# Kernel tuning notes

Hardware: AMD Instinct MI355X
Metric: run time of the kernel (lower is better)

## Reference

```python
import jax, jax.numpy as jnp
import numpy as np
from jax import lax

K_FILTERS = 4
TEMPERATURE = 30.0


def setup_inputs() -> dict:
    key = jax.random.key(0)
    k1, k2, k3, k4 = jax.random.split(key, 4)
    B, C, H, W = 16, 256, 64, 64
    O, Cin, kk = 256, 256, 3
    hidden = int(C * 0.25) + 1  # 65
    x = jax.random.normal(k1, (B, C, H, W), dtype=jnp.float32)
    # kaiming-normal-ish scales for SE 1x1 convs (fan_out, relu)
    fc1_w = jax.random.normal(k2, (hidden, C), dtype=jnp.float32) * np.float32(np.sqrt(2.0 / hidden))
    fc2_w = jax.random.normal(k3, (O * K_FILTERS, hidden), dtype=jnp.float32) * np.float32(np.sqrt(2.0 / (O * K_FILTERS)))
    fc2_b = jnp.zeros((O * K_FILTERS,), dtype=jnp.float32)
    he_std = np.float32(np.sqrt(2.0) * (C * kk * kk) ** (-0.5))
    weight = jax.random.normal(k4, (K_FILTERS, O, Cin, kk, kk), dtype=jnp.float32) * he_std
    return {"x": x, "fc1_w": fc1_w, "fc2_w": fc2_w, "fc2_b": fc2_b, "weight": weight}


def reference(x, fc1_w, fc2_w, fc2_b, weight):
    B, C, H, W = x.shape
    K, O, Cin, kh, kw = weight.shape
    # SE module: global avg pool -> 1x1 conv (fc) -> relu -> 1x1 conv (fc)
    pooled = x.mean(axis=(2, 3))                      # [B, C]
    h = jax.nn.relu(pooled @ fc1_w.T)                 # [B, hidden]
    y = h @ fc2_w.T + fc2_b                           # [B, K*O]
    # softmax over K filters per output channel
    prob = jax.nn.softmax(y.reshape(B, K, O) / TEMPERATURE, axis=1)  # [B, K, O]
    # per-sample aggregated conv weights
    agg = jnp.einsum('bko,kof->bof', prob, weight.reshape(K, O, Cin * kh * kw))
    agg = agg.reshape(B, O, Cin, kh, kw)              # [B, O, Cin, kh, kw]
    # batched conv with per-sample filters (stride=1, padding=1, dilation=1, groups=1)
    def conv_one(xi, wi):
        return lax.conv_general_dilated(
            xi[None], wi, window_strides=(1, 1), padding=[(1, 1), (1, 1)],
            dimension_numbers=('NCHW', 'OIHW', 'NCHW'))[0]
    out = jax.vmap(conv_one)(x, agg)                  # [B, O, H, W]
    return out
```

## Files before the change

### kernel.cpp

```cpp
#include <hip/hip_runtime.h>
#include <hip/hip_bf16.h>
#include <stdint.h>


typedef __bf16 bf16x8 __attribute__((ext_vector_type(8)));
typedef float  f32x4  __attribute__((ext_vector_type(4)));

__device__ __forceinline__ unsigned short f2bf(float f) {
  union { float f; unsigned u; } v; v.f = f;
  return (unsigned short)((v.u + 0x7FFFu + ((v.u >> 16) & 1u)) >> 16);
}

__device__ __forceinline__ void gload16(const void* g, void* l) {
  __builtin_amdgcn_global_load_lds(
      (const __attribute__((address_space(1))) void*)g,
      (__attribute__((address_space(3))) void*)l, 16, 0, 0);
}

#define WAIT_VM(N) do { __builtin_amdgcn_sched_barrier(0); \
  asm volatile("s_waitcnt vmcnt(" #N ")" ::: "memory"); \
  __builtin_amdgcn_sched_barrier(0); } while (0)
#define BARRIER_PIN() do { __builtin_amdgcn_s_barrier(); \
  __builtin_amdgcn_sched_barrier(0); } while (0)

__global__ __launch_bounds__(256) void k_prep(
    const float* __restrict__ x, unsigned short* __restrict__ xn,
    float* __restrict__ pooled_sum) {
  const int bx = blockIdx.x;
  const int y  = bx & 63;
  const int cc = (bx >> 6) & 3;
  const int b  = bx >> 8;
  const int t  = threadIdx.x;
  const int cl = t >> 2;
  const int q  = t & 3;
  const int xs = q * 16;

  const float4* s4 = (const float4*)(x + (((size_t)(b * 256 + cc * 64 + cl) * 64 + y) * 64 + xs));
  float v[16];
#pragma unroll
  for (int i = 0; i < 4; ++i) {
    float4 f = s4[i];
    v[i * 4 + 0] = f.x; v[i * 4 + 1] = f.y; v[i * 4 + 2] = f.z; v[i * 4 + 3] = f.w;
  }
  float s = 0.f;
#pragma unroll
  for (int i = 0; i < 16; ++i) s += v[i];
  s += __shfl_xor(s, 1);
  s += __shfl_xor(s, 2);
  if (q == 0) atomicAdd(&pooled_sum[b * 256 + cc * 64 + cl], s);

  __shared__ unsigned short tile[64][72];
#pragma unroll
  for (int j = 0; j < 16; ++j) tile[xs + j][cl] = f2bf(v[j]);
  __syncthreads();
  const int xp = t >> 2;
  const uint4* ls = (const uint4*)&tile[xp][q * 16];
  uint4 a0 = ls[0], a1 = ls[1];
  uint4* gd = (uint4*)(xn + ((size_t)((b * 64 + y) * 64 + xp) * 256 + cc * 64 + q * 16));
  gd[0] = a0; gd[1] = a1;
}

__global__ __launch_bounds__(256) void k_fc(
    const float* __restrict__ pooled_sum,
    const float* __restrict__ fc1, const float* __restrict__ fc2,
    const float* __restrict__ fc2b, float* __restrict__ prob) {
  const int b = blockIdx.x, t = threadIdx.x;
  __shared__ float p[256];
  __shared__ float h[72];
  __shared__ float yv[1024];
  p[t] = pooled_sum[b * 256 + t] * (1.0f / 4096.0f);
  __syncthreads();
  if (t < 65) {
    float s = 0.f;
    for (int c = 0; c < 256; ++c) s += p[c] * fc1[t * 256 + c];
    h[t] = fmaxf(s, 0.f);
  }
  __syncthreads();
  for (int m = t; m < 1024; m += 256) {
    float s = fc2b[m];
    for (int j = 0; j < 65; ++j) s += h[j] * fc2[m * 65 + j];
    yv[m] = s;
  }
  __syncthreads();
  const float invT = 1.0f / 30.0f;
  float e0 = yv[t] * invT, e1 = yv[256 + t] * invT, e2 = yv[512 + t] * invT, e3 = yv[768 + t] * invT;
  float mx = fmaxf(fmaxf(e0, e1), fmaxf(e2, e3));
  float x0 = expf(e0 - mx), x1 = expf(e1 - mx), x2 = expf(e2 - mx), x3 = expf(e3 - mx);
  float r = 1.0f / (x0 + x1 + x2 + x3);
  prob[(b * 4 + 0) * 256 + t] = x0 * r;
  prob[(b * 4 + 1) * 256 + t] = x1 * r;
  prob[(b * 4 + 2) * 256 + t] = x2 * r;
  prob[(b * 4 + 3) * 256 + t] = x3 * r;
}

__global__ __launch_bounds__(256) void k_agg(
    const float* __restrict__ weight, const float* __restrict__ prob,
    unsigned short* __restrict__ aggT) {
  const int o = blockIdx.x, t = threadIdx.x;
  __shared__ float w[4][2304];
#pragma unroll
  for (int k = 0; k < 4; ++k) {
    const float4* src = (const float4*)(weight + (size_t)(k * 256 + o) * 2304);
    float4* dst = (float4*)w[k];
    for (int j = t; j < 576; j += 256) dst[j] = src[j];
  }
  __syncthreads();
  const int c = t;
  float wv[4][9];
#pragma unroll
  for (int k = 0; k < 4; ++k)
#pragma unroll
    for (int tap = 0; tap < 9; ++tap) wv[k][tap] = w[k][c * 9 + tap];
  for (int b = 0; b < 16; ++b) {
    float p0 = prob[(b * 4 + 0) * 256 + o];
    float p1 = prob[(b * 4 + 1) * 256 + o];
    float p2 = prob[(b * 4 + 2) * 256 + o];
    float p3 = prob[(b * 4 + 3) * 256 + o];
#pragma unroll
    for (int tap = 0; tap < 9; ++tap) {
      float vv = p0 * wv[0][tap] + p1 * wv[1][tap] + p2 * wv[2][tap] + p3 * wv[3][tap];
      aggT[((size_t)(b * 9 + tap) * 256 + o) * 256 + c] = f2bf(vv);
    }
  }
}

__global__ __launch_bounds__(256, 2) void k_conv(
    const unsigned short* __restrict__ xn,
    const unsigned short* __restrict__ aggT,
    const unsigned short* __restrict__ zpage,
    float* __restrict__ out) {
  const int bx0 = blockIdx.x;
  const int bx  = (bx0 & 7) * 128 + (bx0 >> 3);
  const int ot = bx & 1;
  const int yt = (bx >> 1) & 31;
  const int b  = bx >> 6;
  const int y0 = yt * 2;
  const int o0 = ot * 128;
  const int t    = threadIdx.x;
  const int lane = t & 63;
  const int l15  = lane & 15;
  const int lg   = lane >> 4;
  const int wid  = t >> 6;
  const int wm   = wid >> 1;
  const int wn   = wid & 1;

  __shared__ unsigned short xbuf[256 * 64];
  __shared__ unsigned short wbuf[3][128 * 64];

  const f32x4 vzero = {0.f, 0.f, 0.f, 0.f};
  const bf16x8 bzero = {};
  f32x4 acc[4][4];
#pragma unroll
  for (int i = 0; i < 4; ++i)
#pragma unroll
    for (int j = 0; j < 4; ++j) acc[i][j] = vzero;

  const unsigned short* xb = xn + (size_t)b * (64 * 64 * 256);
  const unsigned short* ab = aggT + (size_t)b * (9 * 256 * 256) + (size_t)o0 * 256;

  for (int cc = 0; cc < 4; ++cc) {
    const int c0 = cc * 64;
#pragma unroll
    for (int i = 0; i < 8; ++i) {
      int u = t + i * 256;
      int pos = u >> 3, s = u & 7;
      int rr = pos >> 6, xc = pos & 63;
      int yy = y0 - 1 + rr;
      int sp = (s ^ (pos & 7)) * 8;
      const unsigned short* src = (yy >= 0 && yy < 64)
          ? xb + ((size_t)yy * 64 + xc) * 256 + (c0 + sp)
          : zpage + ((u & 127) * 8);
      gload16(src, &xbuf[u * 8]);
    }
#pragma unroll
    for (int tp = 0; tp < 2; ++tp) {
      unsigned short* dst = wbuf[tp];
      const unsigned short* wsrc = ab + (size_t)tp * (256 * 256) + c0;
#pragma unroll
      for (int i = 0; i < 4; ++i) {
        int u = t + i * 256;
        int o = u >> 3, s = u & 7;
        gload16(wsrc + (size_t)o * 256 + ((s ^ (o & 7)) * 8), &dst[u * 8]);
      }
    }
    WAIT_VM(4);
    BARRIER_PIN();

#pragma unroll
    for (int tap = 0; tap < 9; ++tap) {
      if (tap < 7) {
        unsigned short* dst = wbuf[(tap + 2) % 3];
        const unsigned short* wsrc = ab + (size_t)(tap + 2) * (256 * 256) + c0;
#pragma unroll
        for (int i = 0; i < 4; ++i) {
          int u = t + i * 256;
          int o = u >> 3, s = u & 7;
          gload16(wsrc + (size_t)o * 256 + ((s ^ (o & 7)) * 8), &dst[u * 8]);
        }
      }
      const int kh = tap / 3;
      const int d  = tap % 3 - 1;
      const int prow = (wm + kh) * 64;
      const unsigned short* wb = wbuf[tap % 3];
#pragma unroll
      for (int ku = 0; ku < 2; ++ku) {
        bf16x8 av[4], bv[4];
#pragma unroll
        for (int mf = 0; mf < 4; ++mf) {
          int xsrc = mf * 16 + l15 + d;
          bool valid = (xsrc >= 0) && (xsrc < 64);
          int xcl = min(max(xsrc, 0), 63);
          int pos = prow + xcl;
          int su = (ku * 4 + lg) ^ (pos & 7);
          av[mf] = *(const bf16x8*)&xbuf[pos * 64 + su * 8];
          if (!valid) av[mf] = bzero;
        }
#pragma unroll
        for (int nf = 0; nf < 4; ++nf) {
          int oo = wn * 64 + nf * 16 + l15;
          int su = (ku * 4 + lg) ^ (oo & 7);
          bv[nf] = *(const bf16x8*)&wb[oo * 64 + su * 8];
        }
        __builtin_amdgcn_s_setprio(1);
#pragma unroll
        for (int mf = 0; mf < 4; ++mf)
#pragma unroll
          for (int nf = 0; nf < 4; ++nf)
            acc[mf][nf] = __builtin_amdgcn_mfma_f32_16x16x32_bf16(av[mf], bv[nf], acc[mf][nf], 0, 0, 0);
        __builtin_amdgcn_s_setprio(0);
      }
      if (tap < 7) { WAIT_VM(4); } else { WAIT_VM(0); }
      BARRIER_PIN();
    }
  }

  const int yrow = y0 + wm;
#pragma unroll
  for (int nf = 0; nf < 4; ++nf) {
    int och = o0 + wn * 64 + nf * 16 + l15;
    float* op = out + ((size_t)(b * 256 + och) * 4096) + yrow * 64;
#pragma unroll
    for (int mf = 0; mf < 4; ++mf) {
      int xcb = mf * 16 + lg * 4;
      *(float4*)(op + xcb) = *(float4*)&acc[mf][nf];
    }
  }
}

extern "C" void kernel_launch(void* const* d_in, const int* in_sizes, int n_in,
                              void* d_out, int out_size, void* d_ws, size_t ws_size,
                              hipStream_t stream) {
  (void)in_sizes; (void)n_in; (void)out_size; (void)ws_size;
  const float* x      = (const float*)d_in[0];
  const float* fc1    = (const float*)d_in[1];
  const float* fc2    = (const float*)d_in[2];
  const float* fc2b   = (const float*)d_in[3];
  const float* weight = (const float*)d_in[4];
  float* out = (float*)d_out;

  char* ws = (char*)d_ws;
  unsigned short* zpage  = (unsigned short*)ws;
  float*          pooled = (float*)(ws + 4096);
  float*          prob   = (float*)(ws + 20480);
  unsigned short* aggT   = (unsigned short*)(ws + 131072);
  unsigned short* xnhwc  = (unsigned short*)(ws + 131072 + 18874368);

  hipMemsetAsync(d_ws, 0, 20480, stream);
  k_prep<<<dim3(16 * 4 * 64), dim3(256), 0, stream>>>(x, xnhwc, pooled);
  k_fc  <<<dim3(16),          dim3(256), 0, stream>>>(pooled, fc1, fc2, fc2b, prob);
  k_agg <<<dim3(256),         dim3(256), 0, stream>>>(weight, prob, aggT);
  k_conv<<<dim3(1024),        dim3(256), 0, stream>>>(xnhwc, aggT, zpage, out);
}
```

Measured before the change: 133.0 us.

## Load conv weights directly to registers and double-buffer x tiles; widen prep blocks

The conv kernel no longer stages per-tap weight tiles through LDS. Each wave reads its B fragments straight from global memory into registers, double-buffered across taps, and the x tile is double-buffered in LDS across channel chunks so one barrier per chunk replaces one per tap. The prep kernel now handles all 256 channels per block, packing bf16 pairs into a wider LDS tile and cutting the block count and atomics per block. This trades LDS traffic and barriers for more register pressure and for uncoalesced direct global loads of weights that may not be hidden behind the MFMAs.

```diff
diff --git a/kernel.cpp b/kernel.cpp
--- a/kernel.cpp
+++ b/kernel.cpp
@@ -17,8 +17,8 @@
       (__attribute__((address_space(3))) void*)l, 16, 0, 0);
 }
 
-#define WAIT_VM(N) do { __builtin_amdgcn_sched_barrier(0); \
-  asm volatile("s_waitcnt vmcnt(" #N ")" ::: "memory"); \
+#define WAIT_VM0() do { __builtin_amdgcn_sched_barrier(0); \
+  asm volatile("s_waitcnt vmcnt(0)" ::: "memory"); \
   __builtin_amdgcn_sched_barrier(0); } while (0)
 #define BARRIER_PIN() do { __builtin_amdgcn_s_barrier(); \
   __builtin_amdgcn_sched_barrier(0); } while (0)
@@ -28,36 +28,37 @@
     float* __restrict__ pooled_sum) {
   const int bx = blockIdx.x;
   const int y  = bx & 63;
-  const int cc = (bx >> 6) & 3;
-  const int b  = bx >> 8;
+  const int b  = bx >> 6;
   const int t  = threadIdx.x;
-  const int cl = t >> 2;
-  const int q  = t & 3;
-  const int xs = q * 16;
-
-  const float4* s4 = (const float4*)(x + (((size_t)(b * 256 + cc * 64 + cl) * 64 + y) * 64 + xs));
-  float v[16];
-#pragma unroll
-  for (int i = 0; i < 4; ++i) {
-    float4 f = s4[i];
-    v[i * 4 + 0] = f.x; v[i * 4 + 1] = f.y; v[i * 4 + 2] = f.z; v[i * 4 + 3] = f.w;
-  }
-  float s = 0.f;
-#pragma unroll
-  for (int i = 0; i < 16; ++i) s += v[i];
-  s += __shfl_xor(s, 1);
-  s += __shfl_xor(s, 2);
-  if (q == 0) atomicAdd(&pooled_sum[b * 256 + cc * 64 + cl], s);
-
-  __shared__ unsigned short tile[64][72];
-#pragma unroll
-  for (int j = 0; j < 16; ++j) tile[xs + j][cl] = f2bf(v[j]);
-  __syncthreads();
-  const int xp = t >> 2;
-  const uint4* ls = (const uint4*)&tile[xp][q * 16];
-  uint4 a0 = ls[0], a1 = ls[1];
-  uint4* gd = (uint4*)(xn + ((size_t)((b * 64 + y) * 64 + xp) * 256 + cc * 64 + q * 16));
-  gd[0] = a0; gd[1] = a1;
+  const int c2 = t & 127;
+  const int xh = t >> 7;
+
+  const float4* r0 = (const float4*)(x + (((size_t)(b * 256 + 2 * c2    ) * 64 + y) * 64 + xh * 32));
+  const float4* r1 = (const float4*)(x + (((size_t)(b * 256 + 2 * c2 + 1) * 64 + y) * 64 + xh * 32));
+
+  __shared__ unsigned int tile[64][132];
+
+  float s0 = 0.f, s1 = 0.f;
+#pragma unroll
+  for (int i = 0; i < 8; ++i) {
+    float4 a0 = r0[i], a1 = r1[i];
+    s0 += a0.x + a0.y + a0.z + a0.w;
+    s1 += a1.x + a1.y + a1.z + a1.w;
+    const int xb = xh * 32 + i * 4;
+    tile[xb + 0][c2] = (unsigned)f2bf(a0.x) | ((unsigned)f2bf(a1.x) << 16);
+    tile[xb + 1][c2] = (unsigned)f2bf(a0.y) | ((unsigned)f2bf(a1.y) << 16);
+    tile[xb + 2][c2] = (unsigned)f2bf(a0.z) | ((unsigned)f2bf(a1.z) << 16);
+    tile[xb + 3][c2] = (unsigned)f2bf(a0.w) | ((unsigned)f2bf(a1.w) << 16);
+  }
+  atomicAdd(&pooled_sum[b * 256 + 2 * c2    ], s0);
+  atomicAdd(&pooled_sum[b * 256 + 2 * c2 + 1], s1);
+  __syncthreads();
+
+  const int p = t >> 2, q = t & 3;
+  const uint4* ls = (const uint4*)&tile[p][q * 32];
+  uint4* gd = (uint4*)(xn + ((size_t)((b * 64 + y) * 64 + p) * 256 + q * 64));
+#pragma unroll
+  for (int i = 0; i < 8; ++i) gd[i] = ls[i];
 }
 
 __global__ __launch_bounds__(256) void k_fc(
@@ -144,8 +145,7 @@
   const int wm   = wid >> 1;
   const int wn   = wid & 1;
 
-  __shared__ unsigned short xbuf[256 * 64];
-  __shared__ unsigned short wbuf[3][128 * 64];
+  __shared__ unsigned short xbuf[2][256 * 64];
 
   const f32x4 vzero = {0.f, 0.f, 0.f, 0.f};
   const bf16x8 bzero = {};
@@ -157,9 +157,10 @@
 
   const unsigned short* xb = xn + (size_t)b * (64 * 64 * 256);
   const unsigned short* ab = aggT + (size_t)b * (9 * 256 * 256) + (size_t)o0 * 256;
-
-  for (int cc = 0; cc < 4; ++cc) {
-    const int c0 = cc * 64;
+  const unsigned short* wbase = ab + (size_t)(wn * 64 + l15) * 256 + lg * 8;
+
+  auto stageX = [&](int buf, int cc) {
+    const int c0s = cc * 64;
 #pragma unroll
     for (int i = 0; i < 8; ++i) {
       int u = t + i * 256;
@@ -168,43 +169,47 @@
       int yy = y0 - 1 + rr;
       int sp = (s ^ (pos & 7)) * 8;
       const unsigned short* src = (yy >= 0 && yy < 64)
-          ? xb + ((size_t)yy * 64 + xc) * 256 + (c0 + sp)
+          ? xb + ((size_t)yy * 64 + xc) * 256 + (c0s + sp)
           : zpage + ((u & 127) * 8);
-      gload16(src, &xbuf[u * 8]);
-    }
-#pragma unroll
-    for (int tp = 0; tp < 2; ++tp) {
-      unsigned short* dst = wbuf[tp];
-      const unsigned short* wsrc = ab + (size_t)tp * (256 * 256) + c0;
-#pragma unroll
-      for (int i = 0; i < 4; ++i) {
-        int u = t + i * 256;
-        int o = u >> 3, s = u & 7;
-        gload16(wsrc + (size_t)o * 256 + ((s ^ (o & 7)) * 8), &dst[u * 8]);
-      }
-    }
-    WAIT_VM(4);
-    BARRIER_PIN();
+      gload16(src, &xbuf[buf][u * 8]);
+    }
+  };
+
+  stageX(0, 0);
+  WAIT_VM0();
+  BARRIER_PIN();
+
+  for (int cc = 0; cc < 4; ++cc) {
+    const int c0 = cc * 64;
+    const unsigned short* xcur = xbuf[cc & 1];
+    if (cc < 3) {
+      stageX((cc + 1) & 1, cc + 1);
+      __builtin_amdgcn_sched_barrier(0);
+    }
+
+    bf16x8 bfrag[2][8];
+#pragma unroll
+    for (int nf = 0; nf < 4; ++nf)
+#pragma unroll
+      for (int ku = 0; ku < 2; ++ku)
+        bfrag[0][nf * 2 + ku] = *(const bf16x8*)(wbase + nf * 4096 + c0 + ku * 32);
 
 #pragma unroll
     for (int tap = 0; tap < 9; ++tap) {
-      if (tap < 7) {
-        unsigned short* dst = wbuf[(tap + 2) % 3];
-        const unsigned short* wsrc = ab + (size_t)(tap + 2) * (256 * 256) + c0;
-#pragma unroll
-        for (int i = 0; i < 4; ++i) {
-          int u = t + i * 256;
-          int o = u >> 3, s = u & 7;
-          gload16(wsrc + (size_t)o * 256 + ((s ^ (o & 7)) * 8), &dst[u * 8]);
-        }
+      if (tap < 8) {
+        const unsigned short* wt = wbase + (size_t)(tap + 1) * 65536 + c0;
+#pragma unroll
+        for (int nf = 0; nf < 4; ++nf)
+#pragma unroll
+          for (int ku = 0; ku < 2; ++ku)
+            bfrag[(tap + 1) & 1][nf * 2 + ku] = *(const bf16x8*)(wt + nf * 4096 + ku * 32);
       }
       const int kh = tap / 3;
       const int d  = tap % 3 - 1;
       const int prow = (wm + kh) * 64;
-      const unsigned short* wb = wbuf[tap % 3];
 #pragma unroll
       for (int ku = 0; ku < 2; ++ku) {
-        bf16x8 av[4], bv[4];
+        bf16x8 av[4];
 #pragma unroll
         for (int mf = 0; mf < 4; ++mf) {
           int xsrc = mf * 16 + l15 + d;
@@ -212,26 +217,21 @@
           int xcl = min(max(xsrc, 0), 63);
           int pos = prow + xcl;
           int su = (ku * 4 + lg) ^ (pos & 7);
-          av[mf] = *(const bf16x8*)&xbuf[pos * 64 + su * 8];
+          av[mf] = *(const bf16x8*)&xcur[pos * 64 + su * 8];
           if (!valid) av[mf] = bzero;
         }
-#pragma unroll
-        for (int nf = 0; nf < 4; ++nf) {
-          int oo = wn * 64 + nf * 16 + l15;
-          int su = (ku * 4 + lg) ^ (oo & 7);
-          bv[nf] = *(const bf16x8*)&wb[oo * 64 + su * 8];
-        }
         __builtin_amdgcn_s_setprio(1);
 #pragma unroll
         for (int mf = 0; mf < 4; ++mf)
 #pragma unroll
           for (int nf = 0; nf < 4; ++nf)
-            acc[mf][nf] = __builtin_amdgcn_mfma_f32_16x16x32_bf16(av[mf], bv[nf], acc[mf][nf], 0, 0, 0);
+            acc[mf][nf] = __builtin_amdgcn_mfma_f32_16x16x32_bf16(
+                av[mf], bfrag[tap & 1][nf * 2 + ku], acc[mf][nf], 0, 0, 0);
         __builtin_amdgcn_s_setprio(0);
       }
-      if (tap < 7) { WAIT_VM(4); } else { WAIT_VM(0); }
-      BARRIER_PIN();
-    }
+    }
+    WAIT_VM0();
+    BARRIER_PIN();
   }
 
   const int yrow = y0 + wm;
@@ -266,8 +266,8 @@
   unsigned short* xnhwc  = (unsigned short*)(ws + 131072 + 18874368);
 
   hipMemsetAsync(d_ws, 0, 20480, stream);
-  k_prep<<<dim3(16 * 4 * 64), dim3(256), 0, stream>>>(x, xnhwc, pooled);
-  k_fc  <<<dim3(16),          dim3(256), 0, stream>>>(pooled, fc1, fc2, fc2b, prob);
-  k_agg <<<dim3(256),         dim3(256), 0, stream>>>(weight, prob, aggT);
-  k_conv<<<dim3(1024),        dim3(256), 0, stream>>>(xnhwc, aggT, zpage, out);
-}
+  k_prep<<<dim3(16 * 64),  dim3(256), 0, stream>>>(x, xnhwc, pooled);
+  k_fc  <<<dim3(16),       dim3(256), 0, stream>>>(pooled, fc1, fc2, fc2b, prob);
+  k_agg <<<dim3(256),      dim3(256), 0, stream>>>(weight, prob, aggT);
+  k_conv<<<dim3(1024),     dim3(256), 0, stream>>>(xnhwc, aggT, zpage, out);
+}
```

New measurement: 220.2 us. 65.6% more time.

## Software-pipeline LDS fragment reads ahead of MFMAs across taps and channel chunks

Applied to the files above, without the earlier changes.

Restructures the conv main loop so that the A and B fragments for the next tap are read from LDS while the current tap's MFMAs run, holding all 8 fragments per operand in registers. It also prefetches the next channel chunk's x tile and the first weight taps across the chunk boundary, so the pipeline does not drain and refill at the start of each chunk. The aim is to hide LDS read latency and the per-chunk prologue stalls. In exchange it uses more registers and relies on delicate waitcnt and barrier ordering: the x buffer is overwritten while tap-8 reads are still pending, guarded by an extra lgkmcnt wait and barrier.

```diff
diff --git a/kernel.cpp b/kernel.cpp
--- a/kernel.cpp
+++ b/kernel.cpp
@@ -21,6 +21,8 @@
   asm volatile("s_waitcnt vmcnt(" #N ")" ::: "memory"); \
   __builtin_amdgcn_sched_barrier(0); } while (0)
 #define BARRIER_PIN() do { __builtin_amdgcn_s_barrier(); \
+  __builtin_amdgcn_sched_barrier(0); } while (0)
+#define LGKM0_PIN() do { asm volatile("s_waitcnt lgkmcnt(0)" ::: "memory"); \
   __builtin_amdgcn_sched_barrier(0); } while (0)
 
 __global__ __launch_bounds__(256) void k_prep(
@@ -158,8 +160,18 @@
   const unsigned short* xb = xn + (size_t)b * (64 * 64 * 256);
   const unsigned short* ab = aggT + (size_t)b * (9 * 256 * 256) + (size_t)o0 * 256;
 
-  for (int cc = 0; cc < 4; ++cc) {
-    const int c0 = cc * 64;
+  auto stage_w = [&](int tap, int ccs) {
+    unsigned short* dst = wbuf[tap % 3];
+    const unsigned short* wsrc = ab + (size_t)tap * (256 * 256) + ccs * 64;
+#pragma unroll
+    for (int i = 0; i < 4; ++i) {
+      int u = t + i * 256;
+      int o = u >> 3, s = u & 7;
+      gload16(wsrc + (size_t)o * 256 + ((s ^ (o & 7)) * 8), &dst[u * 8]);
+    }
+  };
+  auto stage_x = [&](int ccs) {
+    const int c0s = ccs * 64;
 #pragma unroll
     for (int i = 0; i < 8; ++i) {
       int u = t + i * 256;
@@ -168,71 +180,99 @@
       int yy = y0 - 1 + rr;
       int sp = (s ^ (pos & 7)) * 8;
       const unsigned short* src = (yy >= 0 && yy < 64)
-          ? xb + ((size_t)yy * 64 + xc) * 256 + (c0 + sp)
+          ? xb + ((size_t)yy * 64 + xc) * 256 + (c0s + sp)
           : zpage + ((u & 127) * 8);
       gload16(src, &xbuf[u * 8]);
     }
-#pragma unroll
-    for (int tp = 0; tp < 2; ++tp) {
-      unsigned short* dst = wbuf[tp];
-      const unsigned short* wsrc = ab + (size_t)tp * (256 * 256) + c0;
-#pragma unroll
-      for (int i = 0; i < 4; ++i) {
-        int u = t + i * 256;
-        int o = u >> 3, s = u & 7;
-        gload16(wsrc + (size_t)o * 256 + ((s ^ (o & 7)) * 8), &dst[u * 8]);
-      }
-    }
-    WAIT_VM(4);
-    BARRIER_PIN();
-
+  };
+
+#define READ_A1(I, KU, MF, TAP) do {                                    \
+    const int kh_ = (TAP) / 3, d_ = (TAP) % 3 - 1;                      \
+    int xsrc_ = (MF) * 16 + l15 + d_;                                   \
+    bool valid_ = (xsrc_ >= 0) && (xsrc_ < 64);                         \
+    int pos_ = (wm + kh_) * 64 + min(max(xsrc_, 0), 63);                \
+    int su_ = ((KU) * 4 + lg) ^ (pos_ & 7);                             \
+    bf16x8 v_ = *(const bf16x8*)&xbuf[pos_ * 64 + su_ * 8];             \
+    av[I] = valid_ ? v_ : bzero;                                        \
+  } while (0)
+#define READ_A_ALL(TAP) do {                                            \
+    READ_A1(0, 0, 0, TAP); READ_A1(1, 0, 1, TAP);                       \
+    READ_A1(2, 0, 2, TAP); READ_A1(3, 0, 3, TAP);                       \
+    READ_A1(4, 1, 0, TAP); READ_A1(5, 1, 1, TAP);                       \
+    READ_A1(6, 1, 2, TAP); READ_A1(7, 1, 3, TAP);                       \
+  } while (0)
+#define READ_B1(I, KU, NF, SLOT) do {                                   \
+    int oo_ = wn * 64 + (NF) * 16 + l15;                                \
+    int su_ = ((KU) * 4 + lg) ^ (oo_ & 7);                              \
+    bv[I] = *(const bf16x8*)&wbuf[SLOT][oo_ * 64 + su_ * 8];            \
+  } while (0)
+#define READ_B_ALL(SLOT) do {                                           \
+    READ_B1(0, 0, 0, SLOT); READ_B1(1, 0, 1, SLOT);                     \
+    READ_B1(2, 0, 2, SLOT); READ_B1(3, 0, 3, SLOT);                     \
+    READ_B1(4, 1, 0, SLOT); READ_B1(5, 1, 1, SLOT);                     \
+    READ_B1(6, 1, 2, SLOT); READ_B1(7, 1, 3, SLOT);                     \
+  } while (0)
+#define MFMA4(AI, KU, MF) do {                                          \
+    acc[MF][0] = __builtin_amdgcn_mfma_f32_16x16x32_bf16(av[AI], bv[(KU)*4+0], acc[MF][0], 0, 0, 0); \
+    acc[MF][1] = __builtin_amdgcn_mfma_f32_16x16x32_bf16(av[AI], bv[(KU)*4+1], acc[MF][1], 0, 0, 0); \
+    acc[MF][2] = __builtin_amdgcn_mfma_f32_16x16x32_bf16(av[AI], bv[(KU)*4+2], acc[MF][2], 0, 0, 0); \
+    acc[MF][3] = __builtin_amdgcn_mfma_f32_16x16x32_bf16(av[AI], bv[(KU)*4+3], acc[MF][3], 0, 0, 0); \
+  } while (0)
+#define MFMA_ALL() do {                                                 \
+    __builtin_amdgcn_s_setprio(1);                                      \
+    MFMA4(0, 0, 0); MFMA4(1, 0, 1); MFMA4(2, 0, 2); MFMA4(3, 0, 3);     \
+    MFMA4(4, 1, 0); MFMA4(5, 1, 1); MFMA4(6, 1, 2); MFMA4(7, 1, 3);     \
+    __builtin_amdgcn_s_setprio(0);                                      \
+  } while (0)
+
+  bf16x8 av[8], bv[8];
+
+  stage_x(0);
+  stage_w(0, 0);
+  stage_w(1, 0);
+  WAIT_VM(4);
+  BARRIER_PIN();
+  READ_B_ALL(0);
+  READ_A_ALL(0);
+
+  for (int cc = 0; cc < 4; ++cc) {
 #pragma unroll
     for (int tap = 0; tap < 9; ++tap) {
+      if (tap == 8 && cc < 3) stage_x(cc + 1);
+      if (cc < 3 || tap <= 6) stage_w((tap + 2) % 9, cc + (tap + 2) / 9);
+
+      MFMA_ALL();
+
       if (tap < 7) {
-        unsigned short* dst = wbuf[(tap + 2) % 3];
-        const unsigned short* wsrc = ab + (size_t)(tap + 2) * (256 * 256) + c0;
-#pragma unroll
-        for (int i = 0; i < 4; ++i) {
-          int u = t + i * 256;
-          int o = u >> 3, s = u & 7;
-          gload16(wsrc + (size_t)o * 256 + ((s ^ (o & 7)) * 8), &dst[u * 8]);
+        READ_A_ALL(tap + 1);
+        WAIT_VM(4);
+        BARRIER_PIN();
+        READ_B_ALL((tap + 1) % 3);
+      } else if (tap == 7) {
+        READ_A_ALL(8);
+        if (cc < 3) { WAIT_VM(4); } else { WAIT_VM(0); }
+        BARRIER_PIN();
+        READ_B_ALL(2);
+        if (cc < 3) {
+          LGKM0_PIN();
+          BARRIER_PIN();
+        }
+      } else {
+        if (cc < 3) {
+          WAIT_VM(4);
+          BARRIER_PIN();
+          READ_B_ALL(0);
+          READ_A_ALL(0);
         }
       }
-      const int kh = tap / 3;
-      const int d  = tap % 3 - 1;
-      const int prow = (wm + kh) * 64;
-      const unsigned short* wb = wbuf[tap % 3];
-#pragma unroll
-      for (int ku = 0; ku < 2; ++ku) {
-        bf16x8 av[4], bv[4];
-#pragma unroll
-        for (int mf = 0; mf < 4; ++mf) {
-          int xsrc = mf * 16 + l15 + d;
-          bool valid = (xsrc >= 0) && (xsrc < 64);
-          int xcl = min(max(xsrc, 0), 63);
-          int pos = prow + xcl;
-          int su = (ku * 4 + lg) ^ (pos & 7);
-          av[mf] = *(const bf16x8*)&xbuf[pos * 64 + su * 8];
-          if (!valid) av[mf] = bzero;
-        }
-#pragma unroll
-        for (int nf = 0; nf < 4; ++nf) {
-          int oo = wn * 64 + nf * 16 + l15;
-          int su = (ku * 4 + lg) ^ (oo & 7);
-          bv[nf] = *(const bf16x8*)&wb[oo * 64 + su * 8];
-        }
-        __builtin_amdgcn_s_setprio(1);
-#pragma unroll
-        for (int mf = 0; mf < 4; ++mf)
-#pragma unroll
-          for (int nf = 0; nf < 4; ++nf)
-            acc[mf][nf] = __builtin_amdgcn_mfma_f32_16x16x32_bf16(av[mf], bv[nf], acc[mf][nf], 0, 0, 0);
-        __builtin_amdgcn_s_setprio(0);
-      }
-      if (tap < 7) { WAIT_VM(4); } else { WAIT_VM(0); }
-      BARRIER_PIN();
-    }
-  }
+    }
+  }
+#undef READ_A1
+#undef READ_A_ALL
+#undef READ_B1
+#undef READ_B_ALL
+#undef MFMA4
+#undef MFMA_ALL
 
   const int yrow = y0 + wm;
 #pragma unroll
```

Measured after the change: 134.8 us. No clear change (+1.4%).
